# Performance work log

Hardware: AMD Instinct MI355X
Metric: run time of the kernel (lower is better)

The kernel has to match this reference:

```python
import jax, jax.numpy as jnp
import numpy as np

MAX_SHIFT_BANDS = 2.0


def setup_inputs() -> dict:
    key = jax.random.key(0)
    k1, k2 = jax.random.split(key)
    B, Bh, H, W = 4, 128, 256, 256
    x = jax.random.normal(k1, (B, Bh, H, W), dtype=jnp.float32)
    wavelength_shift = jax.random.normal(k2, (B, Bh, W), dtype=jnp.float32)
    return {"x": x, "wavelength_shift": wavelength_shift}


def reference(x, wavelength_shift):
    # Faithful to torch grid_sample(mode='bilinear', padding_mode='border',
    # align_corners=False) applied along the spectral (band) axis only.
    B, Bh, H, W = x.shape
    dt = x.dtype

    shift = jnp.clip(wavelength_shift, -MAX_SHIFT_BANDS, MAX_SHIFT_BANDS)
    shift = shift[:, :, None, :]                         # [B,Bh,1,W]
    band = jnp.arange(Bh, dtype=dt)[None, :, None, None]  # [1,Bh,1,1]
    shifted = jnp.clip(band + shift, 0.0, Bh - 1)        # [B,Bh,1,W]

    # grid_sample align_corners=False unnormalization:
    # grid g = shifted/(Bh-1)*2 - 1 ; iy = ((g+1)*Bh - 1)/2 = shifted*Bh/(Bh-1) - 0.5
    iy = shifted * (Bh / (Bh - 1)) - 0.5                 # [B,Bh,1,W]
    i0f = jnp.floor(iy)
    w = iy - i0f                                          # lerp weight, [B,Bh,1,W]
    i0 = i0f.astype(jnp.int32)                            # may be -1 at low edge
    i0c = jnp.clip(i0, 0, Bh - 1)                         # border padding
    i1c = jnp.clip(i0 + 1, 0, Bh - 1)

    # broadcast gather indices over H rows
    i0c = jnp.broadcast_to(i0c, (B, Bh, H, W))
    i1c = jnp.broadcast_to(i1c, (B, Bh, H, W))

    x0 = jnp.take_along_axis(x, i0c, axis=1)              # [B,Bh,H,W]
    x1 = jnp.take_along_axis(x, i1c, axis=1)
    return x0 * (1.0 - w) + x1 * w
```

## Files before the change

### kernel.cpp

```cpp
#include <hip/hip_runtime.h>


#define BH_ 128
#define H_  256
#define W_  256
#define TB   16
#define NLDS (TB + 6)

__global__ __launch_bounds__(256) void smile_kernel(
    const float* __restrict__ x,
    const float* __restrict__ ws,
    float* __restrict__ out)
{
    __shared__ float tile[NLDS][W_];

    const int t = threadIdx.x;
    int bid = blockIdx.x;
    const int tileI = bid & 7;
    bid >>= 3;
    const int h = bid & (H_ - 1);
    const int b = bid >> 8;
    const int bh0 = tileI * TB;

    const float* __restrict__ xsrc = x + (size_t)b * (BH_ * H_ * W_) + h * W_;
    const int wave = t >> 6;
    const int lane = t & 63;
    for (int i = wave; i < NLDS; i += 4) {
        const int band = min(max(bh0 - 3 + i, 0), BH_ - 1);
        const float* gp = xsrc + (size_t)band * (H_ * W_) + lane * 4;
        __builtin_amdgcn_global_load_lds(
            (const __attribute__((address_space(1))) void*)gp,
            (__attribute__((address_space(3))) void*)&tile[i][0],
            16, 0, 0);
    }
    __syncthreads();

    const float scale = (float)(128.0 / 127.0);
    const int w = t;
    const float* __restrict__ wsb = ws + (size_t)(b * BH_ + bh0) * W_ + w;
    float* __restrict__ outb =
        out + (((size_t)b * BH_ + bh0) * H_ + h) * W_ + w;

    float s[TB];
#pragma unroll
    for (int r = 0; r < TB; ++r)
        s[r] = wsb[r * W_];

#pragma unroll
    for (int r = 0; r < TB; ++r) {
        const int bh = bh0 + r;
        float sc      = fminf(fmaxf(s[r], -2.0f), 2.0f);
        float shifted = fminf(fmaxf((float)bh + sc, 0.0f), (float)(BH_ - 1));
        float iy      = fmaf(shifted, scale, -0.5f);
        float i0f     = floorf(iy);
        float frac    = iy - i0f;
        int   i0      = (int)i0f;
        int   r0      = min(max(i0, 0), BH_ - 1) - bh0 + 3;
        int   r1      = min(i0 + 1, BH_ - 1) - bh0 + 3;
        float x0 = tile[r0][w];
        float x1 = tile[r1][w];
        outb[(size_t)r * (H_ * W_)] = fmaf(frac, x1 - x0, x0);
    }
}

extern "C" void kernel_launch(void* const* d_in, const int* in_sizes, int n_in,
                              void* d_out, int out_size, void* d_ws, size_t ws_size,
                              hipStream_t stream) {
    const float* x  = (const float*)d_in[0];
    const float* ws = (const float*)d_in[1];
    float* out = (float*)d_out;

    const int grid = 4 * H_ * (BH_ / TB);
    smile_kernel<<<grid, 256, 0, stream>>>(x, ws, out);
}
```

Baseline: 50.65 us.

## Give each wave a private LDS band tile and drop block-wide barrier

Each wave now loads its own 22-row by 64-column slice of bands into a private LDS region with 4-byte global_load_lds and waits only on its own vmcnt, which removes the block-wide __syncthreads. Blocks are remapped so that one block covers two band groups by four waves, and block IDs are swizzled across XCDs. Output stores become nontemporal, and launch bounds request 7 blocks per CU. In exchange, the direct-to-LDS loads are narrower (4 bytes per lane instead of 16), which issues more load instructions, and the waves of a block no longer share halo rows.

Result: faster. 45.44 us (-10.3%).

```diff
diff --git a/kernel.cpp b/kernel.cpp
--- a/kernel.cpp
+++ b/kernel.cpp
@@ -4,62 +4,73 @@
 #define BH_ 128
 #define H_  256
 #define W_  256
-#define TB   16
-#define NLDS (TB + 6)
+#define BG   16
+#define NR   22
 
-__global__ __launch_bounds__(256) void smile_kernel(
+__global__ __launch_bounds__(256, 7) void smile_kernel(
     const float* __restrict__ x,
     const float* __restrict__ ws,
     float* __restrict__ out)
 {
-    __shared__ float tile[NLDS][W_];
+    __shared__ float tile[4][NR * 64];
 
-    const int t = threadIdx.x;
-    int bid = blockIdx.x;
-    const int tileI = bid & 7;
-    bid >>= 3;
-    const int h = bid & (H_ - 1);
-    const int b = bid >> 8;
-    const int bh0 = tileI * TB;
+    const int t    = threadIdx.x;
+    const int wv   = t >> 6;
+    const int lane = t & 63;
 
-    const float* __restrict__ xsrc = x + (size_t)b * (BH_ * H_ * W_) + h * W_;
-    const int wave = t >> 6;
-    const int lane = t & 63;
-    for (int i = wave; i < NLDS; i += 4) {
+    const int bid0 = blockIdx.x;
+    const int bid  = (bid0 & 7) * 1024 + (bid0 >> 3);
+
+    const int bgb = bid & 1;
+    int rem = bid >> 1;
+    const int wg  = rem & 3;
+    rem >>= 2;
+    const int h   = rem & (H_ - 1);
+    const int b   = rem >> 8;
+
+    const int bg  = bgb * 4 + wv;
+    const int bh0 = bg * BG;
+    const int w   = wg * 64 + lane;
+
+    float* const tl = &tile[wv][0];
+
+#pragma unroll
+    for (int i = 0; i < NR; ++i) {
         const int band = min(max(bh0 - 3 + i, 0), BH_ - 1);
-        const float* gp = xsrc + (size_t)band * (H_ * W_) + lane * 4;
+        const float* gp = x + ((size_t)(b * BH_ + band) * H_ + h) * W_ + w;
         __builtin_amdgcn_global_load_lds(
             (const __attribute__((address_space(1))) void*)gp,
-            (__attribute__((address_space(3))) void*)&tile[i][0],
-            16, 0, 0);
+            (__attribute__((address_space(3))) void*)&tl[i * 64],
+            4, 0, 0);
     }
-    __syncthreads();
+
+    const float* __restrict__ wsp = ws + (size_t)(b * BH_ + bh0) * W_ + w;
+    float s[BG];
+#pragma unroll
+    for (int r = 0; r < BG; ++r)
+        s[r] = wsp[r * W_];
+
+    asm volatile("s_waitcnt vmcnt(0)" ::: "memory");
 
     const float scale = (float)(128.0 / 127.0);
-    const int w = t;
-    const float* __restrict__ wsb = ws + (size_t)(b * BH_ + bh0) * W_ + w;
-    float* __restrict__ outb =
-        out + (((size_t)b * BH_ + bh0) * H_ + h) * W_ + w;
-
-    float s[TB];
-#pragma unroll
-    for (int r = 0; r < TB; ++r)
-        s[r] = wsb[r * W_];
+    float* __restrict__ outp =
+        out + ((size_t)(b * BH_ + bh0) * H_ + h) * W_ + w;
 
 #pragma unroll
-    for (int r = 0; r < TB; ++r) {
-        const int bh = bh0 + r;
+    for (int r = 0; r < BG; ++r) {
+        const int bh  = bh0 + r;
         float sc      = fminf(fmaxf(s[r], -2.0f), 2.0f);
         float shifted = fminf(fmaxf((float)bh + sc, 0.0f), (float)(BH_ - 1));
         float iy      = fmaf(shifted, scale, -0.5f);
         float i0f     = floorf(iy);
         float frac    = iy - i0f;
         int   i0      = (int)i0f;
-        int   r0      = min(max(i0, 0), BH_ - 1) - bh0 + 3;
-        int   r1      = min(i0 + 1, BH_ - 1) - bh0 + 3;
-        float x0 = tile[r0][w];
-        float x1 = tile[r1][w];
-        outb[(size_t)r * (H_ * W_)] = fmaf(frac, x1 - x0, x0);
+        int   r0      = min(max(i0, 0), BH_ - 1) - (bh0 - 3);
+        int   r1      = min(i0 + 1, BH_ - 1) - (bh0 - 3);
+        float x0 = tl[r0 * 64 + lane];
+        float x1 = tl[r1 * 64 + lane];
+        __builtin_nontemporal_store(fmaf(frac, x1 - x0, x0),
+                                    outp + (size_t)r * (H_ * W_));
     }
 }
 
@@ -70,6 +81,6 @@
     const float* ws = (const float*)d_in[1];
     float* out = (float*)d_out;
 
-    const int grid = 4 * H_ * (BH_ / TB);
+    const int grid = 8192;
     smile_kernel<<<grid, 256, 0, stream>>>(x, ws, out);
 }
```
